# Kernel tuning notes

Measured on AMD Instinct MI355X. Metric: run time of the kernel, lower is better.

## Reference

```python
import jax, jax.numpy as jnp
import numpy as np

N_S, N_RT, N_SHP, N_EXP = 1, 11, 50, 29
TOP_K, N_OBJS = 32, 32
IOU_THR = 0.4
RESIZE = 160.0
RAD2DEG = 180.0 / np.pi


def _nms_single(boxes, scores):
    # boxes: (N,4) [y1,x1,y2,x2]; scores: (N,). Greedy class-agnostic NMS
    # replicating tf.image.combined_non_max_suppression with c=1 and zero padding.
    N = scores.shape[0]
    order = jnp.argsort(-scores)
    b = boxes[order]
    s = scores[order]
    area = (b[:, 2] - b[:, 0]) * (b[:, 3] - b[:, 1])
    yy1 = jnp.maximum(b[:, None, 0], b[None, :, 0])
    xx1 = jnp.maximum(b[:, None, 1], b[None, :, 1])
    yy2 = jnp.minimum(b[:, None, 2], b[None, :, 2])
    xx2 = jnp.minimum(b[:, None, 3], b[None, :, 3])
    inter = jnp.clip(yy2 - yy1, 0.0) * jnp.clip(xx2 - xx1, 0.0)
    union = area[:, None] + area[None, :] - inter
    iou = jax.lax.stop_gradient(inter / jnp.maximum(union, 1e-8))
    idxs = jnp.arange(N)

    def body(i, supp):
        row = (iou[i] > IOU_THR) & (idxs > i) & jnp.logical_not(supp[i])
        return supp | row

    supp = jax.lax.fori_loop(0, N, body, jnp.zeros((N,), bool))
    keep = ~supp
    rank = jnp.cumsum(keep) - 1
    valid = keep & (rank < N_OBJS)
    slot = jnp.where(valid, rank, N_OBJS)  # out-of-range -> dropped
    ob = jnp.zeros((N_OBJS, 4), b.dtype).at[slot].set(b, mode='drop')
    osc = jnp.zeros((N_OBJS,), s.dtype).at[slot].set(s, mode='drop')
    ocl = jnp.zeros((N_OBJS,), s.dtype)  # single class -> class 0
    return ob, osc, ocl


def _forward(hms, pmaps, origin_shapes, pms, u_base, shp_base, exp_base):
    B, H, W, C = hms.shape  # C == 1
    resize_ratio = origin_shapes / RESIZE  # (B,2) [ry, rx]
    # keep-local-maxima via 3x3 max pool (Base.apply_max_pool)
    pooled = jax.lax.reduce_window(hms, -np.inf, jax.lax.max,
                                   (1, 3, 3, 1), (1, 1, 1, 1), 'SAME')
    peaks = jnp.where(pooled == hms, hms, 0.0)
    flat = peaks.reshape(B, H * W)
    scores, idx = jax.lax.top_k(flat, TOP_K)  # (B,N)
    ys, xs = idx // W, idx % W
    bidx = jnp.arange(B)[:, None]
    params = pmaps[bidx, ys, xs]  # (B,N,91) gather_nd
    mask = scores > 0.5  # score gating (literal 0.5 as in source)
    params = params * pms[1] + pms[0]
    s = params[..., :N_S]
    Rt = params[..., N_S:N_S + N_RT]
    shp = params[..., N_S + N_RT:N_S + N_RT + N_SHP]
    exp = params[..., N_S + N_RT + N_SHP:]
    # 3DMM vertices: (B,N,204) -> (B,N,68,3); u_base already mean-centered
    verts = (u_base[:, 0][None, None, :]
             + jnp.einsum('vp,bnp->bnv', shp_base, shp)
             + jnp.einsum('vp,bnp->bnv', exp_base, exp))
    verts = verts.reshape(B, TOP_K, 68, 3)
    Rt = jnp.concatenate([Rt, jnp.ones((B, TOP_K, 1), Rt.dtype)], -1)
    Rt = Rt.reshape(B, TOP_K, 3, 4)
    R = Rt[..., :3]  # (B,N,3,3); t column is unused (as in source)
    lnmks = s[..., None] * jnp.einsum('bnvc,bnrc->bnvr', verts, R)  # verts @ R^T
    coors = jnp.stack([ys, xs], -1).astype(jnp.float32) * resize_ratio[:, None, :]
    coors_xy = coors[..., ::-1]
    lnmks_yx = (lnmks[..., :2] + coors_xy[:, :, None, :])[..., ::-1]  # (B,N,68,2)
    tls = lnmks_yx.min(axis=2)
    brs = lnmks_yx.max(axis=2)
    bboxes = jnp.concatenate([tls, brs, scores[..., None]], -1)  # (B,N,5)
    bboxes = jnp.where(mask[..., None], bboxes, -1.0)  # invalid slots stay -1
    nb, ns, ncl = jax.vmap(_nms_single)(bboxes[..., :4], bboxes[..., 4])
    box_results = jnp.where(nb == -1.0, jnp.inf, nb)
    box_results = jnp.where(box_results == 0.0, jnp.inf, box_results)
    out_bboxes = jnp.concatenate([box_results, ns[..., None], ncl[..., None]], -1)
    # _valid_lnmks: match NMS-kept detections back to candidates by score equality
    det_valid = jnp.all(out_bboxes != jnp.inf, axis=-1)  # (B,M)
    eq = (scores[:, :, None] == ns[:, None, :]) & det_valid[:, None, :]
    matched = eq.any(-1)  # (B,N)
    lnmks_flat = lnmks_yx.reshape(B, TOP_K, 68 * 2)
    out_lnmks = jnp.where(matched[..., None], lnmks_flat, -1.0)
    out_lnmks = out_lnmks.reshape(B, N_OBJS, 68, 2)
    yaw = jnp.arcsin(-R[..., 2, 0]) * RAD2DEG
    cy = jnp.cos(yaw)  # cosine of DEGREES value, faithful to the original code
    pitch = jnp.arctan2(R[..., 2, 1] / cy, R[..., 2, 2] / cy) * RAD2DEG
    roll = jnp.arctan2(R[..., 1, 0] / cy, R[..., 0, 0] / cy) * RAD2DEG
    pose = jnp.stack([pitch, yaw, roll], -1)  # (B,N,3)
    out_pose = jnp.where(matched[..., None], pose, -1.0)
    out_lnmks = jnp.where(out_lnmks == -1.0, jnp.inf, out_lnmks)
    out_pose = jnp.where(out_pose == -1.0, jnp.inf, out_pose)
    return out_bboxes, out_lnmks, out_pose


def setup_inputs() -> dict:
    key = jax.random.key(0)
    ks = jax.random.split(key, 5)
    B, H, W = 16, 160, 160
    hms = jax.random.uniform(ks[0], (B, H, W, 1), jnp.float32)
    pmaps = jax.random.normal(ks[1], (B, H, W, 91), jnp.float32)
    origin_shapes = jnp.full((B, 2), 640.0, jnp.float32)  # 640px originals
    mean = np.zeros(91, np.float32)
    mean[0] = 0.001  # 3DMM scale
    mean[1:12] = np.array([1, 0, 0, 0, 0, 1, 0, 0, 0, 0, 1], np.float32)  # ~identity Rt
    std = np.full(91, 0.02, np.float32)
    pms = jnp.asarray(np.stack([mean, std]))  # (2,91): row0 mean, row1 std
    u = jax.random.normal(ks[2], (68, 3), jnp.float32) * 100.0
    u = u - u.mean(axis=0, keepdims=True)  # mean-centered as in __init__
    u_base = u.reshape(204, 1)
    shp_base = jax.random.normal(ks[3], (204, 50), jnp.float32)
    exp_base = jax.random.normal(ks[4], (204, 29), jnp.float32)
    return {"hms": hms, "pmaps": pmaps, "origin_shapes": origin_shapes,
            "pms": pms, "u_base": u_base, "shp_base": shp_base,
            "exp_base": exp_base}


def reference(hms, pmaps, origin_shapes, pms, u_base, shp_base, exp_base):
    return _forward(hms, pmaps, origin_shapes, pms, u_base, shp_base, exp_base)
```

## Files before the change

kernel.cpp:

```cpp
#include <hip/hip_runtime.h>
#include <math.h>

#define HW   25600
#define WID  160
#define NPAR 91
#define TOPK 32
#define NCH  20
#define NCAND (NCH*TOPK)

#define CV_OFF 0
#define CI_OFF 10240
#define TV_OFF 20480
#define TI_OFF 20992
#define BB_OFF 21504
#define PS_OFF 24064
#define LN_OFF 25600

__global__ __launch_bounds__(256) void k1_peaks(const float* __restrict__ hms,
                                                float* __restrict__ wsf,
                                                int* __restrict__ wsi)
{
  const int chunk = blockIdx.x;
  const int b     = blockIdx.y;
  const int tid   = threadIdx.x;
  const float* hb = hms + (size_t)b * HW;

  __shared__ float tile[10 * 160];
  __shared__ float cv[384];
  __shared__ int   ci[384];
  __shared__ int   cnt;
  if (tid == 0) cnt = 0;

  for (int i = tid; i < 400; i += 256) {
    int r = i / 40, g = i - 40 * r;
    int gr = chunk * 8 - 1 + r;
    float4 val;
    if (gr < 0 || gr >= 160) val = make_float4(-INFINITY, -INFINITY, -INFINITY, -INFINITY);
    else                     val = *(const float4*)(hb + gr * WID + g * 4);
    *(float4*)(tile + r * 160 + g * 4) = val;
  }
  __syncthreads();

  #pragma unroll
  for (int k = 0; k < 5; ++k) {
    int lp = tid + (k << 8);
    int y  = lp / 160, x = lp - y * 160;
    int ty = y + 1;
    float c = tile[ty * 160 + x];
    bool peak = true;
    if (x > 0) {
      if (tile[(ty - 1) * 160 + x - 1] > c) peak = false;
      if (tile[ ty      * 160 + x - 1] > c) peak = false;
      if (tile[(ty + 1) * 160 + x - 1] > c) peak = false;
    }
    if (tile[(ty - 1) * 160 + x] > c) peak = false;
    if (tile[(ty + 1) * 160 + x] > c) peak = false;
    if (x < 159) {
      if (tile[(ty - 1) * 160 + x + 1] > c) peak = false;
      if (tile[ ty      * 160 + x + 1] > c) peak = false;
      if (tile[(ty + 1) * 160 + x + 1] > c) peak = false;
    }
    if (peak || lp < 32) {
      int slot = atomicAdd(&cnt, 1);
      cv[slot] = peak ? c : 0.0f;
      ci[slot] = chunk * 1280 + lp;
    }
  }
  __syncthreads();

  const int P = cnt;
  float* outv = wsf + CV_OFF + b * NCAND + chunk * TOPK;
  int*   outi = wsi + CI_OFF + b * NCAND + chunk * TOPK;
  for (int j = tid; j < P; j += 256) {
    float vj = cv[j]; int ij = ci[j];
    int rank = 0;
    for (int m = 0; m < P; ++m) {
      float vm = cv[m]; int im = ci[m];
      rank += (vm > vj || (vm == vj && im < ij)) ? 1 : 0;
    }
    if (rank < TOPK) { outv[rank] = vj; outi[rank] = ij; }
  }
}

__global__ __launch_bounds__(256) void k2_topk(float* __restrict__ wsf,
                                               int* __restrict__ wsi)
{
  const int seg = blockIdx.x;
  const int b   = blockIdx.y;
  const int tid = threadIdx.x;

  __shared__ float cv[NCAND];
  __shared__ int   ci[NCAND];
  const float* inv = wsf + CV_OFF + b * NCAND;
  const int*   ini = wsi + CI_OFF + b * NCAND;
  for (int j = tid; j < NCAND; j += 256) { cv[j] = inv[j]; ci[j] = ini[j]; }
  __syncthreads();

  if (tid < 160) {
    int j = seg * 160 + tid;
    float vj = cv[j]; int ij = ci[j];
    int rank = 0;
    for (int m = 0; m < NCAND; ++m) {
      float vm = cv[m]; int im = ci[m];
      rank += (vm > vj || (vm == vj && im < ij)) ? 1 : 0;
    }
    if (rank < TOPK) {
      wsf[TV_OFF + b * TOPK + rank] = vj;
      wsi[TI_OFF + b * TOPK + rank] = ij;
    }
  }
}

__global__ __launch_bounds__(256) void k3_verts(const float* __restrict__ pmaps,
                                                const float* __restrict__ oshapes,
                                                const float* __restrict__ pms,
                                                const float* __restrict__ ub,
                                                const float* __restrict__ sb,
                                                const float* __restrict__ eb,
                                                float* __restrict__ wsf,
                                                const int* __restrict__ wsi)
{
  const int n   = blockIdx.x;
  const int b   = blockIdx.y;
  const int tid = threadIdx.x;

  __shared__ float s_sb[10200];
  __shared__ float s_eb[5916];
  __shared__ float s_ub[204];
  __shared__ float s_prm[NPAR];
  __shared__ float s_v[204];
  __shared__ float s_pyx[136];

  {
    const float4* s4 = (const float4*)sb;
    float4* d4 = (float4*)s_sb;
    for (int i = tid; i < 2550; i += 256) d4[i] = s4[i];
    const float4* e4 = (const float4*)eb;
    float4* de = (float4*)s_eb;
    for (int i = tid; i < 1479; i += 256) de[i] = e4[i];
    if (tid < 51) ((float4*)s_ub)[tid] = ((const float4*)ub)[tid];
  }
  const int p = wsi[TI_OFF + b * TOPK + n];
  if (tid < NPAR)
    s_prm[tid] = pmaps[((size_t)b * HW + p) * NPAR + tid] * pms[NPAR + tid] + pms[tid];
  __syncthreads();

  if (tid < 204) {
    float acc = s_ub[tid];
    const float* srow = s_sb + tid * 50;
    for (int q = 0; q < 50; ++q) acc += srow[q] * s_prm[12 + q];
    const float* erow = s_eb + tid * 29;
    for (int q = 0; q < 29; ++q) acc += erow[q] * s_prm[62 + q];
    s_v[tid] = acc;
  }
  __syncthreads();

  const int ys = p / WID, xs = p - (p / WID) * WID;
  if (tid < 68) {
    float a0 = s_v[3 * tid], a1 = s_v[3 * tid + 1], a2 = s_v[3 * tid + 2];
    float s  = s_prm[0];
    float l0 = s * (a0 * s_prm[1] + a1 * s_prm[2] + a2 * s_prm[3]);
    float l1 = s * (a0 * s_prm[5] + a1 * s_prm[6] + a2 * s_prm[7]);
    float rr0 = oshapes[2 * b]     / 160.0f;
    float rr1 = oshapes[2 * b + 1] / 160.0f;
    float py = l1 + (float)ys * rr0;
    float px = l0 + (float)xs * rr1;
    float* ln = wsf + LN_OFF + ((size_t)b * TOPK + n) * 136;
    ln[2 * tid]     = py;
    ln[2 * tid + 1] = px;
    s_pyx[2 * tid]     = py;
    s_pyx[2 * tid + 1] = px;
  }
  __syncthreads();

  if (tid < 64) {
    float py = s_pyx[2 * tid], px = s_pyx[2 * tid + 1];
    float mny = py, mxy = py, mnx = px, mxx = px;
    if (tid < 4) {
      float qy = s_pyx[128 + 2 * tid], qx = s_pyx[129 + 2 * tid];
      mny = fminf(mny, qy); mxy = fmaxf(mxy, qy);
      mnx = fminf(mnx, qx); mxx = fmaxf(mxx, qx);
    }
    #pragma unroll
    for (int off = 32; off > 0; off >>= 1) {
      mny = fminf(mny, __shfl_xor(mny, off));
      mnx = fminf(mnx, __shfl_xor(mnx, off));
      mxy = fmaxf(mxy, __shfl_xor(mxy, off));
      mxx = fmaxf(mxx, __shfl_xor(mxx, off));
    }
    if (tid == 0) {
      float sc = wsf[TV_OFF + b * TOPK + n];
      bool mask = sc > 0.5f;
      float* bb = wsf + BB_OFF + ((size_t)b * TOPK + n) * 5;
      bb[0] = mask ? mny : -1.0f;
      bb[1] = mask ? mnx : -1.0f;
      bb[2] = mask ? mxy : -1.0f;
      bb[3] = mask ? mxx : -1.0f;
      bb[4] = mask ? sc  : -1.0f;
      const float R2D = 57.29577951308232f;
      float R20 = s_prm[9], R21 = s_prm[10], R22 = s_prm[11];
      float yaw = asinf(-R20) * R2D;
      float cyw = cosf(yaw);
      float pitch = atan2f(R21 / cyw, R22 / cyw) * R2D;
      float roll  = atan2f(s_prm[5] / cyw, s_prm[1] / cyw) * R2D;
      float* ps = wsf + PS_OFF + ((size_t)b * TOPK + n) * 3;
      ps[0] = pitch; ps[1] = yaw; ps[2] = roll;
    }
  }
}

__global__ __launch_bounds__(256) void k4_nms(const float* __restrict__ wsf,
                                              float* __restrict__ out)
{
  const int b   = blockIdx.x;
  const int tid = threadIdx.x;

  __shared__ float s_bbox[TOPK][5];
  __shared__ float s_topv[TOPK];
  __shared__ float s_obox[TOPK][4];
  __shared__ float s_osc[TOPK];
  __shared__ int   s_dv[TOPK];
  __shared__ int   s_match[TOPK];

  if (tid < 160) ((float*)s_bbox)[tid] = wsf[BB_OFF + b * 160 + tid];
  if (tid < TOPK) s_topv[tid] = wsf[TV_OFF + b * TOPK + tid];
  __syncthreads();

  if (tid < 64) {
    int j = tid;
    float b0 = 0.f, b1 = 0.f, b2 = 0.f, b3 = 0.f, sc = -1e30f;
    if (j < TOPK) {
      b0 = s_bbox[j][0]; b1 = s_bbox[j][1]; b2 = s_bbox[j][2]; b3 = s_bbox[j][3];
      sc = s_bbox[j][4];
    }
    float area = (b2 - b0) * (b3 - b1);
    int supp = (j >= TOPK) ? 1 : 0;
    for (int i = 0; i < TOPK; ++i) {
      float i0 = __shfl(b0, i), i1 = __shfl(b1, i);
      float i2 = __shfl(b2, i), i3 = __shfl(b3, i);
      float ia = __shfl(area, i);
      int isup = __shfl(supp, i);
      if (!isup && j > i && j < TOPK) {
        float yy1 = fmaxf(b0, i0), xx1 = fmaxf(b1, i1);
        float yy2 = fminf(b2, i2), xx2 = fminf(b3, i3);
        float inter = fmaxf(yy2 - yy1, 0.0f) * fmaxf(xx2 - xx1, 0.0f);
        float uni = area + ia - inter;
        float iou = inter / fmaxf(uni, 1e-8f);
        if (iou > 0.4f) supp = 1;
      }
    }
    bool keep = (j < TOPK) && !supp;
    unsigned long long km = __ballot(keep);
    int rank = __popcll(km & ((1ull << j) - 1ull));
    if (j < TOPK) {
      s_obox[j][0] = 0.f; s_obox[j][1] = 0.f; s_obox[j][2] = 0.f; s_obox[j][3] = 0.f;
      s_osc[j] = 0.f;
    }
    if (keep) {
      s_obox[rank][0] = b0; s_obox[rank][1] = b1;
      s_obox[rank][2] = b2; s_obox[rank][3] = b3;
      s_osc[rank] = sc;
    }
  }
  __syncthreads();

  if (tid < TOPK) {
    int dv = 1;
    #pragma unroll
    for (int c = 0; c < 4; ++c) {
      float t = s_obox[tid][c];
      if (t == -1.0f || t == 0.0f) { t = INFINITY; dv = 0; }
      s_obox[tid][c] = t;
    }
    s_dv[tid] = dv;
  }
  __syncthreads();

  if (tid < TOPK) {
    float mysc = s_topv[tid];
    int m = 0;
    for (int sl = 0; sl < TOPK; ++sl)
      if (s_dv[sl] && s_osc[sl] == mysc) m = 1;
    s_match[tid] = m;
  }
  __syncthreads();

  {
    float* outb = out + (size_t)b * 192;
    for (int j = tid; j < 192; j += 256) {
      int sl = j / 6, c = j - 6 * sl;
      float val;
      if (c < 4)       val = s_obox[sl][c];
      else if (c == 4) val = s_osc[sl];
      else             val = 0.0f;
      outb[j] = val;
    }
    const float* lnw = wsf + LN_OFF + (size_t)b * (TOPK * 136);
    float* outl = out + 3072 + (size_t)b * 4352;
    for (int j = tid; j < 4352; j += 256) {
      int n = j / 136;
      float t = lnw[j];
      outl[j] = s_match[n] ? ((t == -1.0f) ? INFINITY : t) : INFINITY;
    }
    const float* psw = wsf + PS_OFF + (size_t)b * (TOPK * 3);
    float* outp = out + 72704 + (size_t)b * 96;
    for (int j = tid; j < 96; j += 256) {
      int n = j / 3;
      float t = psw[j];
      outp[j] = s_match[n] ? ((t == -1.0f) ? INFINITY : t) : INFINITY;
    }
  }
}

extern "C" void kernel_launch(void* const* d_in, const int* in_sizes, int n_in,
                              void* d_out, int out_size, void* d_ws, size_t ws_size,
                              hipStream_t stream) {
  const float* hms   = (const float*)d_in[0];
  const float* pmaps = (const float*)d_in[1];
  const float* osh   = (const float*)d_in[2];
  const float* pms   = (const float*)d_in[3];
  const float* ub    = (const float*)d_in[4];
  const float* sb    = (const float*)d_in[5];
  const float* eb    = (const float*)d_in[6];
  float* o   = (float*)d_out;
  float* wsf = (float*)d_ws;
  int*   wsi = (int*)d_ws;

  k1_peaks<<<dim3(NCH, 16), 256, 0, stream>>>(hms, wsf, wsi);
  k2_topk <<<dim3(4, 16),  256, 0, stream>>>(wsf, wsi);
  k3_verts<<<dim3(32, 16), 256, 0, stream>>>(pmaps, osh, pms, ub, sb, eb, wsf, wsi);
  k4_nms  <<<16,           256, 0, stream>>>(wsf, o);
}
```

Baseline: 241.3 us.

## Fuse four kernels into two using last-block atomic counters

Merges the chunk top-k and global top-k kernels, and the vertex and NMS kernels, into two kernels. In each, the last block to finish for a batch (found with an atomic counter after a threadfence) runs the follow-on reduction. This removes two kernel launches and their inter-kernel gaps. It adds a memset launch for the counters, and the merged top-k now runs in a single block per batch rather than four.

```diff
diff --git a/kernel.cpp b/kernel.cpp
--- a/kernel.cpp
+++ b/kernel.cpp
@@ -15,8 +15,10 @@
 #define BB_OFF 21504
 #define PS_OFF 24064
 #define LN_OFF 25600
-
-__global__ __launch_bounds__(256) void k1_peaks(const float* __restrict__ hms,
+#define CT1_OFF 95232
+#define CT2_OFF 95248
+
+__global__ __launch_bounds__(256) void kA_peaks(const float* __restrict__ hms,
                                                 float* __restrict__ wsf,
                                                 int* __restrict__ wsi)
 {
@@ -29,6 +31,7 @@
   __shared__ float cv[384];
   __shared__ int   ci[384];
   __shared__ int   cnt;
+  __shared__ int   lastf;
   if (tid == 0) cnt = 0;
 
   for (int i = tid; i < 400; i += 256) {
@@ -80,28 +83,28 @@
     }
     if (rank < TOPK) { outv[rank] = vj; outi[rank] = ij; }
   }
-}
-
-__global__ __launch_bounds__(256) void k2_topk(float* __restrict__ wsf,
-                                               int* __restrict__ wsi)
-{
-  const int seg = blockIdx.x;
-  const int b   = blockIdx.y;
-  const int tid = threadIdx.x;
-
-  __shared__ float cv[NCAND];
-  __shared__ int   ci[NCAND];
+
+  __threadfence();
+  __syncthreads();
+  if (tid == 0) {
+    int old = atomicAdd(wsi + CT1_OFF + b, 1);
+    lastf = (old == NCH - 1);
+  }
+  __syncthreads();
+  if (!lastf) return;
+  __threadfence();
+
+  __shared__ float cv2[NCAND];
+  __shared__ int   ci2[NCAND];
   const float* inv = wsf + CV_OFF + b * NCAND;
   const int*   ini = wsi + CI_OFF + b * NCAND;
-  for (int j = tid; j < NCAND; j += 256) { cv[j] = inv[j]; ci[j] = ini[j]; }
-  __syncthreads();
-
-  if (tid < 160) {
-    int j = seg * 160 + tid;
-    float vj = cv[j]; int ij = ci[j];
+  for (int j = tid; j < NCAND; j += 256) { cv2[j] = inv[j]; ci2[j] = ini[j]; }
+  __syncthreads();
+  for (int j = tid; j < NCAND; j += 256) {
+    float vj = cv2[j]; int ij = ci2[j];
     int rank = 0;
     for (int m = 0; m < NCAND; ++m) {
-      float vm = cv[m]; int im = ci[m];
+      float vm = cv2[m]; int im = ci2[m];
       rank += (vm > vj || (vm == vj && im < ij)) ? 1 : 0;
     }
     if (rank < TOPK) {
@@ -111,14 +114,15 @@
   }
 }
 
-__global__ __launch_bounds__(256) void k3_verts(const float* __restrict__ pmaps,
-                                                const float* __restrict__ oshapes,
-                                                const float* __restrict__ pms,
-                                                const float* __restrict__ ub,
-                                                const float* __restrict__ sb,
-                                                const float* __restrict__ eb,
-                                                float* __restrict__ wsf,
-                                                const int* __restrict__ wsi)
+__global__ __launch_bounds__(256) void kB_tail(const float* __restrict__ pmaps,
+                                               const float* __restrict__ oshapes,
+                                               const float* __restrict__ pms,
+                                               const float* __restrict__ ub,
+                                               const float* __restrict__ sb,
+                                               const float* __restrict__ eb,
+                                               float* __restrict__ wsf,
+                                               int* __restrict__ wsi,
+                                               float* __restrict__ out)
 {
   const int n   = blockIdx.x;
   const int b   = blockIdx.y;
@@ -130,6 +134,7 @@
   __shared__ float s_prm[NPAR];
   __shared__ float s_v[204];
   __shared__ float s_pyx[136];
+  __shared__ int   lastf;
 
   {
     const float4* s4 = (const float4*)sb;
@@ -207,13 +212,16 @@
       ps[0] = pitch; ps[1] = yaw; ps[2] = roll;
     }
   }
-}
-
-__global__ __launch_bounds__(256) void k4_nms(const float* __restrict__ wsf,
-                                              float* __restrict__ out)
-{
-  const int b   = blockIdx.x;
-  const int tid = threadIdx.x;
+
+  __threadfence();
+  __syncthreads();
+  if (tid == 0) {
+    int old = atomicAdd(wsi + CT2_OFF + b, 1);
+    lastf = (old == TOPK - 1);
+  }
+  __syncthreads();
+  if (!lastf) return;
+  __threadfence();
 
   __shared__ float s_bbox[TOPK][5];
   __shared__ float s_topv[TOPK];
@@ -298,16 +306,16 @@
     const float* lnw = wsf + LN_OFF + (size_t)b * (TOPK * 136);
     float* outl = out + 3072 + (size_t)b * 4352;
     for (int j = tid; j < 4352; j += 256) {
-      int n = j / 136;
+      int nn = j / 136;
       float t = lnw[j];
-      outl[j] = s_match[n] ? ((t == -1.0f) ? INFINITY : t) : INFINITY;
+      outl[j] = s_match[nn] ? ((t == -1.0f) ? INFINITY : t) : INFINITY;
     }
     const float* psw = wsf + PS_OFF + (size_t)b * (TOPK * 3);
     float* outp = out + 72704 + (size_t)b * 96;
     for (int j = tid; j < 96; j += 256) {
-      int n = j / 3;
+      int nn = j / 3;
       float t = psw[j];
-      outp[j] = s_match[n] ? ((t == -1.0f) ? INFINITY : t) : INFINITY;
+      outp[j] = s_match[nn] ? ((t == -1.0f) ? INFINITY : t) : INFINITY;
     }
   }
 }
@@ -326,8 +334,8 @@
   float* wsf = (float*)d_ws;
   int*   wsi = (int*)d_ws;
 
-  k1_peaks<<<dim3(NCH, 16), 256, 0, stream>>>(hms, wsf, wsi);
-  k2_topk <<<dim3(4, 16),  256, 0, stream>>>(wsf, wsi);
-  k3_verts<<<dim3(32, 16), 256, 0, stream>>>(pmaps, osh, pms, ub, sb, eb, wsf, wsi);
-  k4_nms  <<<16,           256, 0, stream>>>(wsf, o);
+  hipMemsetAsync((char*)d_ws + CT1_OFF * 4, 0, 32 * 4, stream);
+
+  kA_peaks<<<dim3(NCH, 16), 256, 0, stream>>>(hms, wsf, wsi);
+  kB_tail <<<dim3(32, 16),  256, 0, stream>>>(pmaps, osh, pms, ub, sb, eb, wsf, wsi, o);
 }
```

Result: slower. 333.4 us (+38.2%).

## Fuse top-k merge into vertex kernel and drop shared-memory basis staging

Applied to the files above, without the earlier changes.

Removes the separate k2_topk launch. Each k3_verts block now redundantly recomputes the global top-32 ranking over the 640 per-chunk candidates in shared memory and takes its own index and score from that result. Block n==0 alone writes the top scores to the workspace for later use. It also stops copying the ~64KB shape and expression bases into shared memory and reads them straight from global/L2. That cuts the shared-memory footprint and the staging work, but adds redundant ranking work and uncoalesced strided global reads in each block.

```diff
diff --git a/kernel.cpp b/kernel.cpp
--- a/kernel.cpp
+++ b/kernel.cpp
@@ -11,7 +11,6 @@
 #define CV_OFF 0
 #define CI_OFF 10240
 #define TV_OFF 20480
-#define TI_OFF 20992
 #define BB_OFF 21504
 #define PS_OFF 24064
 #define LN_OFF 25600
@@ -79,35 +78,6 @@
       rank += (vm > vj || (vm == vj && im < ij)) ? 1 : 0;
     }
     if (rank < TOPK) { outv[rank] = vj; outi[rank] = ij; }
-  }
-}
-
-__global__ __launch_bounds__(256) void k2_topk(float* __restrict__ wsf,
-                                               int* __restrict__ wsi)
-{
-  const int seg = blockIdx.x;
-  const int b   = blockIdx.y;
-  const int tid = threadIdx.x;
-
-  __shared__ float cv[NCAND];
-  __shared__ int   ci[NCAND];
-  const float* inv = wsf + CV_OFF + b * NCAND;
-  const int*   ini = wsi + CI_OFF + b * NCAND;
-  for (int j = tid; j < NCAND; j += 256) { cv[j] = inv[j]; ci[j] = ini[j]; }
-  __syncthreads();
-
-  if (tid < 160) {
-    int j = seg * 160 + tid;
-    float vj = cv[j]; int ij = ci[j];
-    int rank = 0;
-    for (int m = 0; m < NCAND; ++m) {
-      float vm = cv[m]; int im = ci[m];
-      rank += (vm > vj || (vm == vj && im < ij)) ? 1 : 0;
-    }
-    if (rank < TOPK) {
-      wsf[TV_OFF + b * TOPK + rank] = vj;
-      wsi[TI_OFF + b * TOPK + rank] = ij;
-    }
   }
 }
 
@@ -124,32 +94,43 @@
   const int b   = blockIdx.y;
   const int tid = threadIdx.x;
 
-  __shared__ float s_sb[10200];
-  __shared__ float s_eb[5916];
-  __shared__ float s_ub[204];
+  __shared__ float cv2[NCAND];
+  __shared__ int   ci2[NCAND];
+  __shared__ float s_tv[TOPK];
+  __shared__ int   s_ti[TOPK];
   __shared__ float s_prm[NPAR];
   __shared__ float s_v[204];
   __shared__ float s_pyx[136];
 
-  {
-    const float4* s4 = (const float4*)sb;
-    float4* d4 = (float4*)s_sb;
-    for (int i = tid; i < 2550; i += 256) d4[i] = s4[i];
-    const float4* e4 = (const float4*)eb;
-    float4* de = (float4*)s_eb;
-    for (int i = tid; i < 1479; i += 256) de[i] = e4[i];
-    if (tid < 51) ((float4*)s_ub)[tid] = ((const float4*)ub)[tid];
-  }
-  const int p = wsi[TI_OFF + b * TOPK + n];
+  const float* inv = wsf + CV_OFF + b * NCAND;
+  const int*   ini = wsi + CI_OFF + b * NCAND;
+  for (int j = tid; j < NCAND; j += 256) { cv2[j] = inv[j]; ci2[j] = ini[j]; }
+  __syncthreads();
+  for (int j = tid; j < NCAND; j += 256) {
+    float vj = cv2[j]; int ij = ci2[j];
+    int rank = 0;
+    for (int m = 0; m < NCAND; ++m) {
+      float vm = cv2[m]; int im = ci2[m];
+      rank += (vm > vj || (vm == vj && im < ij)) ? 1 : 0;
+    }
+    if (rank < TOPK) {
+      s_tv[rank] = vj; s_ti[rank] = ij;
+      if (n == 0) wsf[TV_OFF + b * TOPK + rank] = vj;
+    }
+  }
+  __syncthreads();
+
+  const int   p  = s_ti[n];
+  const float sc = s_tv[n];
   if (tid < NPAR)
     s_prm[tid] = pmaps[((size_t)b * HW + p) * NPAR + tid] * pms[NPAR + tid] + pms[tid];
   __syncthreads();
 
   if (tid < 204) {
-    float acc = s_ub[tid];
-    const float* srow = s_sb + tid * 50;
+    float acc = ub[tid];
+    const float* srow = sb + (size_t)tid * 50;
     for (int q = 0; q < 50; ++q) acc += srow[q] * s_prm[12 + q];
-    const float* erow = s_eb + tid * 29;
+    const float* erow = eb + (size_t)tid * 29;
     for (int q = 0; q < 29; ++q) acc += erow[q] * s_prm[62 + q];
     s_v[tid] = acc;
   }
@@ -189,7 +170,6 @@
       mxx = fmaxf(mxx, __shfl_xor(mxx, off));
     }
     if (tid == 0) {
-      float sc = wsf[TV_OFF + b * TOPK + n];
       bool mask = sc > 0.5f;
       float* bb = wsf + BB_OFF + ((size_t)b * TOPK + n) * 5;
       bb[0] = mask ? mny : -1.0f;
@@ -327,7 +307,6 @@
   int*   wsi = (int*)d_ws;
 
   k1_peaks<<<dim3(NCH, 16), 256, 0, stream>>>(hms, wsf, wsi);
-  k2_topk <<<dim3(4, 16),  256, 0, stream>>>(wsf, wsi);
   k3_verts<<<dim3(32, 16), 256, 0, stream>>>(pmaps, osh, pms, ub, sb, eb, wsf, wsi);
   k4_nms  <<<16,           256, 0, stream>>>(wsf, o);
 }
```

Measured after the change: 270.9 us. 1.12x slower.
